# Optimization experiments

Measured on AMD Instinct MI355X. Metric: run time of the kernel, lower is better.

Reference implementation:

```python
import jax, jax.numpy as jnp
import numpy as np

B, S, D, H = 4, 2048, 1024, 16
HD = D // H


def setup_inputs() -> dict:
    key = jax.random.key(0)
    ks = jax.random.split(key, 12)
    sc = 1.0 / np.sqrt(D)
    return {
        "x": jax.random.normal(ks[0], (B, S, D), dtype=jnp.float32),
        "key_padding_mask": jax.random.randint(ks[1], (B, S), 0, 2).astype(bool),
        "attn_mask_modifier": jax.random.uniform(ks[2], (B, S, S), dtype=jnp.float32),
        "Wq": jax.random.normal(ks[3], (D, D), dtype=jnp.float32) * sc,
        "bq": jax.random.normal(ks[4], (D,), dtype=jnp.float32) * sc,
        "Wk": jax.random.normal(ks[5], (D, D), dtype=jnp.float32) * sc,
        "bk": jax.random.normal(ks[6], (D,), dtype=jnp.float32) * sc,
        "Wv": jax.random.normal(ks[7], (D, D), dtype=jnp.float32) * sc,
        "bv": jax.random.normal(ks[8], (D,), dtype=jnp.float32) * sc,
        "Wo": jax.random.normal(ks[9], (D, D), dtype=jnp.float32) * sc,
        "bo": jax.random.normal(ks[10], (D,), dtype=jnp.float32) * sc,
    }


def reference(x, key_padding_mask, attn_mask_modifier, Wq, bq, Wk, bk, Wv, bv, Wo, bo):
    b, s, d = x.shape
    hd = d // H
    # QKV projections -> [b, H, s, hd]
    q = (x @ Wq + bq).reshape(b, s, H, hd).transpose(0, 2, 1, 3)
    k = (x @ Wk + bk).reshape(b, s, H, hd).transpose(0, 2, 1, 3)
    v = (x @ Wv + bv).reshape(b, s, H, hd).transpose(0, 2, 1, 3)
    energy = jnp.einsum("bhqd,bhkd->bhqk", q, k) / jnp.sqrt(jnp.asarray(hd, x.dtype))
    # handle_neg=False path: multiplicative mask modifier, broadcast over heads
    energy = energy * attn_mask_modifier[:, None, :, :]
    # key_padding_mask is applied on the QUERY axis (unsqueeze(1).unsqueeze(-1)) per source
    energy = jnp.where(key_padding_mask[:, None, :, None], jnp.asarray(-1e10, x.dtype), energy)
    attn = jax.nn.softmax(energy, axis=-1)
    out = jnp.einsum("bhqk,bhkd->bhqd", attn, v).transpose(0, 2, 1, 3).reshape(b, s, d)
    return out @ Wo + bo
```

## Files before the change

### kernel.cpp

```cpp
#include <hip/hip_runtime.h>
#include <cstddef>

constexpr int Bn  = 4;
constexpr int Sn  = 2048;
constexpr int Dn  = 1024;
constexpr int Hn  = 16;
constexpr int HDn = 64;

typedef __bf16 bf16;
typedef __attribute__((ext_vector_type(8))) __bf16 bf16x8;
typedef __attribute__((ext_vector_type(4))) __bf16 bf16x4;
typedef __attribute__((ext_vector_type(4))) float  f32x4;

typedef __attribute__((address_space(1))) const void gvoid;
typedef __attribute__((address_space(3))) void lvoid;

__global__ __launch_bounds__(256) void conv_f32_bf16_k(
    const float* __restrict__ in, bf16* __restrict__ out, int n)
{
    int i = (blockIdx.x * 256 + threadIdx.x) * 4;
    if (i + 3 < n) {
        float4 v = *(const float4*)(in + i);
        bf16 o[4] = {(bf16)v.x, (bf16)v.y, (bf16)v.z, (bf16)v.w};
        *(ulong1*)(out + i) = *(ulong1*)o;
    }
}

__global__ __launch_bounds__(256) void bias_cat_k(
    const float* __restrict__ bq, const float* __restrict__ bk,
    const float* __restrict__ bv, float* __restrict__ o)
{
    const int i = blockIdx.x * 256 + threadIdx.x;
    if (i < 1024)      o[i] = bq[i];
    else if (i < 2048) o[i] = bk[i - 1024];
    else if (i < 3072) o[i] = bv[i - 2048];
}

__global__ __launch_bounds__(256) void conv_wt_k(
    const float* __restrict__ w0, const float* __restrict__ w1,
    const float* __restrict__ w2, const float* __restrict__ w3,
    bf16* __restrict__ o0, bf16* __restrict__ o1,
    bf16* __restrict__ o2, bf16* __restrict__ o3)
{
    const float* W = (blockIdx.z == 0) ? w0 : (blockIdx.z == 1) ? w1
                   : (blockIdx.z == 2) ? w2 : w3;
    bf16* O = (blockIdx.z == 0) ? o0 : (blockIdx.z == 1) ? o1
            : (blockIdx.z == 2) ? o2 : o3;
    __shared__ float t[64][65];
    const int tid = threadIdx.x;
    const int k0 = blockIdx.x * 64;
    const int n0 = blockIdx.y * 64;
    #pragma unroll
    for (int p = 0; p < 16; ++p) {
        const int idx = p * 256 + tid;
        const int r = idx >> 6, c = idx & 63;
        t[r][c] = W[(size_t)(k0 + r) * Dn + n0 + c];
    }
    __syncthreads();
    #pragma unroll
    for (int p = 0; p < 16; ++p) {
        const int idx = p * 256 + tid;
        const int r = idx >> 6, c = idx & 63;
        O[(size_t)(n0 + r) * Dn + k0 + c] = (bf16)t[c][r];
    }
}

#define GEMM_STAGE(Ap, Bp, k0, boff)                                          \
    {                                                                         \
        _Pragma("unroll")                                                     \
        for (int j = 0; j < 4; ++j) {                                         \
            const int rbase = (w * 4 + j) * 8;                                \
            const int r = rbase + srow;                                       \
            __builtin_amdgcn_global_load_lds(                                 \
                (gvoid*)(Ap + (size_t)(m0 + r) * Dn + (k0) + scol),           \
                (lvoid*)&smem[(boff) + rbase * 64], 16, 0, 0);                \
            __builtin_amdgcn_global_load_lds(                                 \
                (gvoid*)(Bp + (size_t)(n0 + r) * Dn + (k0) + scol),           \
                (lvoid*)&smem[(boff) + 128 * 64 + rbase * 64], 16, 0, 0);     \
        }                                                                     \
    }

#define GEMM_COMPUTE(boff)                                                    \
    {                                                                         \
        _Pragma("unroll")                                                     \
        for (int ks = 0; ks < 64; ks += 32) {                                 \
            bf16x8 af[4], bfr[4];                                             \
            _Pragma("unroll")                                                 \
            for (int fm = 0; fm < 4; ++fm)                                    \
                af[fm] = *(const bf16x8*)&smem[(boff) +                       \
                    (wm * 64 + fm * 16 + l15) * 64 + ks + quad * 8];          \
            _Pragma("unroll")                                                 \
            for (int fn = 0; fn < 4; ++fn)                                    \
                bfr[fn] = *(const bf16x8*)&smem[(boff) + 128 * 64 +           \
                    (wn * 64 + fn * 16 + l15) * 64 + ks + quad * 8];          \
            _Pragma("unroll")                                                 \
            for (int fm = 0; fm < 4; ++fm)                                    \
                _Pragma("unroll")                                             \
                for (int fn = 0; fn < 4; ++fn)                                \
                    acc[fm][fn] = __builtin_amdgcn_mfma_f32_16x16x32_bf16(    \
                        af[fm], bfr[fn], acc[fm][fn], 0, 0, 0);               \
        }                                                                     \
    }

#define GEMM_KLOOP(Ap, Bp)                                                    \
    GEMM_STAGE(Ap, Bp, 0, 0);                                                 \
    int boff = 0;                                                             \
    for (int kt = 0; kt < Dn / 64; ++kt) {                                    \
        if (kt + 1 < Dn / 64) {                                               \
            GEMM_STAGE(Ap, Bp, (kt + 1) * 64, boff ^ BUF);                    \
            asm volatile("s_waitcnt vmcnt(8)" ::: "memory");                  \
        } else {                                                              \
            asm volatile("s_waitcnt vmcnt(0)" ::: "memory");                  \
        }                                                                     \
        __builtin_amdgcn_s_barrier();                                         \
        __builtin_amdgcn_sched_barrier(0);                                    \
        GEMM_COMPUTE(boff);                                                   \
        __builtin_amdgcn_sched_barrier(0);                                    \
        __builtin_amdgcn_s_barrier();                                         \
        boff ^= BUF;                                                          \
    }

constexpr int BUF = 2 * 128 * 64;

__global__ __launch_bounds__(256) void gemm_out_k(
    const bf16* __restrict__ A, const bf16* __restrict__ Bt,
    const float* __restrict__ bias, float* __restrict__ outv)
{
    __shared__ __align__(16) bf16 smem[2 * BUF];

    const int tid  = threadIdx.x;
    const int w    = tid >> 6;
    const int lane = tid & 63;
    const int quad = lane >> 4;
    const int l15  = lane & 15;
    const int m0   = blockIdx.x * 128;
    const int n0   = blockIdx.y * 128;
    const int wm   = w >> 1;
    const int wn   = w & 1;
    const int srow = lane >> 3;
    const int scol = (lane & 7) * 8;

    f32x4 acc[4][4] = {};

    GEMM_KLOOP(A, Bt);

    #pragma unroll
    for (int fn = 0; fn < 4; ++fn) {
        const int c = n0 + wn * 64 + fn * 16 + l15;
        const float bv = bias[c];
        #pragma unroll
        for (int fm = 0; fm < 4; ++fm)
            #pragma unroll
            for (int i = 0; i < 4; ++i) {
                const int m = m0 + wm * 64 + fm * 16 + quad * 4 + i;
                outv[(size_t)m * Dn + c] = acc[fm][fn][i] + bv;
            }
    }
}

__global__ __launch_bounds__(256) void gemm_qkv_k(
    const bf16* __restrict__ A, const bf16* __restrict__ Wt,
    const float* __restrict__ bias, bf16* __restrict__ qout,
    bf16* __restrict__ kout, bf16* __restrict__ vout, float scq)
{
    __shared__ __align__(16) bf16 smem[2 * BUF];

    const int tid  = threadIdx.x;
    const int w    = tid >> 6;
    const int lane = tid & 63;
    const int quad = lane >> 4;
    const int l15  = lane & 15;
    const int m0   = blockIdx.x * 128;
    const int n0   = blockIdx.y * 128;
    const int wm   = w >> 1;
    const int wn   = w & 1;
    const int srow = lane >> 3;
    const int scol = (lane & 7) * 8;

    f32x4 acc[4][4] = {};

    GEMM_KLOOP(A, Wt);

    const int sec = n0 >> 10;
    const int cb  = n0 & 1023;

    if (sec < 2) {
        bf16* const outp = sec ? kout : qout;
        const float scale = sec ? 1.0f : scq;
        #pragma unroll
        for (int fn = 0; fn < 4; ++fn) {
            const int cc = cb + wn * 64 + fn * 16 + l15;
            const float bv = bias[n0 + wn * 64 + fn * 16 + l15];
            const int h = cc >> 6, hd = cc & 63;
            #pragma unroll
            for (int fm = 0; fm < 4; ++fm)
                #pragma unroll
                for (int i = 0; i < 4; ++i) {
                    const int m = m0 + wm * 64 + fm * 16 + quad * 4 + i;
                    const int b = m >> 11, s = m & (Sn - 1);
                    outp[(((size_t)(b * Hn + h) * Sn) + s) * HDn + hd] =
                        (bf16)((acc[fm][fn][i] + bv) * scale);
                }
        }
    } else {
        bf16* const T = smem;
        #pragma unroll
        for (int fn = 0; fn < 4; ++fn) {
            const int n = wn * 64 + fn * 16 + l15;
            const float bv = bias[n0 + n];
            #pragma unroll
            for (int fm = 0; fm < 4; ++fm) {
                const int m = wm * 64 + fm * 16 + quad * 4;
                bf16x4 pk;
                #pragma unroll
                for (int i = 0; i < 4; ++i)
                    pk[i] = (bf16)(acc[fm][fn][i] + bv);
                *(bf16x4*)&T[n * 136 + m] = pk;
            }
        }
        __syncthreads();
        const int b  = m0 >> 11;
        const int s0 = m0 & (Sn - 1);
        #pragma unroll
        for (int it = 0; it < 8; ++it) {
            const int n    = it * 16 + (tid >> 4);
            const int mcol = (tid & 15) * 8;
            const int gh = (cb + n) >> 6, ghd = (cb + n) & 63;
            bf16x8 v = *(const bf16x8*)&T[n * 136 + mcol];
            *(bf16x8*)(vout +
                (((size_t)(b * Hn + gh) * HDn) + ghd) * Sn + s0 + mcol) = v;
        }
    }
}

__device__ __forceinline__ int sidx(int r, int c) {
    return r * 64 + (c ^ ((r & 7) << 3));
}

__global__ __launch_bounds__(512, 6) void attn_mfma_k(
    const bf16* __restrict__ Qb, const bf16* __restrict__ Kb,
    const bf16* __restrict__ Vtb, const int* __restrict__ kpm,
    const float* __restrict__ mod, bf16* __restrict__ att)
{
    __shared__ __align__(16) bf16 Ks[2][64 * 64];
    __shared__ __align__(16) bf16 Vts[2][64 * 64];
    __shared__ __align__(16) bf16 Ps[128 * 64];

    const int tid  = threadIdx.x;
    const int w    = tid >> 6;
    const int lane = tid & 63;
    const int quad = lane >> 4;
    const int l15  = lane & 15;
    const int blk  = blockIdx.x;
    const int bh   = blk >> 4;
    const int q0   = (blk & 15) * 128;
    const int b    = bh >> 4;
    const int h    = bh & 15;
    const size_t base = (size_t)bh * Sn * HDn;

    const int qrow = q0 + w * 16 + l15;
    const bf16x8 qf0 = *(const bf16x8*)(Qb + base + (size_t)qrow * HDn + 0  + quad * 8);
    const bf16x8 qf1 = *(const bf16x8*)(Qb + base + (size_t)qrow * HDn + 32 + quad * 8);

    const float qbias = (kpm[(size_t)b * Sn + qrow] != 0) ? -1e30f : 0.0f;
    const float* modrow = mod + ((size_t)b * Sn + qrow) * Sn;

    float m_r = -1e30f;
    float l_r = 0.0f;
    f32x4 O[4] = {};

    const int rl = lane >> 3;
    const int cg = ((lane & 7) ^ rl) * 8;
    const int gb = w * 8;

    auto stage = [&](int t, int buf) {
        const int k0 = t * 64;
        __builtin_amdgcn_global_load_lds(
            (gvoid*)(Kb + base + (size_t)(k0 + gb + rl) * HDn + cg),
            (lvoid*)&Ks[buf][gb * 64], 16, 0, 0);
        __builtin_amdgcn_global_load_lds(
            (gvoid*)(Vtb + base + (size_t)(gb + rl) * Sn + k0 + cg),
            (lvoid*)&Vts[buf][gb * 64], 16, 0, 0);
    };

    stage(0, 0);
    float4 md[4];
    #pragma unroll
    for (int ct = 0; ct < 4; ++ct)
        md[ct] = *(const float4*)(modrow + ct * 16 + quad * 4);
    __syncthreads();

    constexpr int NT = Sn / 64;
    for (int t = 0; t < NT; ++t) {
        const int cur = t & 1;

        float4 mdn[4];
        if (t + 1 < NT) {
            stage(t + 1, cur ^ 1);
            #pragma unroll
            for (int ct = 0; ct < 4; ++ct)
                mdn[ct] = *(const float4*)(modrow + (t + 1) * 64 + ct * 16 + quad * 4);
        }

        float e[4][4];
        #pragma unroll
        for (int ct = 0; ct < 4; ++ct) {
            f32x4 s = {};
            #pragma unroll
            for (int ks = 0; ks < 64; ks += 32) {
                bf16x8 kf = *(const bf16x8*)&Ks[cur][sidx(ct * 16 + l15, ks + quad * 8)];
                s = __builtin_amdgcn_mfma_f32_16x16x32_bf16(kf, ks ? qf1 : qf0, s, 0, 0, 0);
            }
            #pragma unroll
            for (int i = 0; i < 4; ++i)
                e[ct][i] = fmaf(s[i], (&md[ct].x)[i], qbias);
        }

        float pm[4];
        #pragma unroll
        for (int ct = 0; ct < 4; ++ct)
            pm[ct] = fmaxf(fmaxf(e[ct][0], e[ct][1]), fmaxf(e[ct][2], e[ct][3]));
        float pmax = fmaxf(fmaxf(pm[0], pm[1]), fmaxf(pm[2], pm[3]));
        pmax = fmaxf(pmax, __shfl_xor(pmax, 16));
        pmax = fmaxf(pmax, __shfl_xor(pmax, 32));

        if (__any(pmax > m_r + 8.0f)) {
            const float mnew  = fmaxf(m_r, pmax);
            const float alpha = __builtin_amdgcn_exp2f(m_r - mnew);
            m_r = mnew;
            l_r *= alpha;
            float aO[4];
            #pragma unroll
            for (int i = 0; i < 4; ++i)
                aO[i] = __shfl(alpha, quad * 4 + i, 16);
            #pragma unroll
            for (int ct = 0; ct < 4; ++ct)
                #pragma unroll
                for (int i = 0; i < 4; ++i)
                    O[ct][i] *= aO[i];
        }

        float rsc[4];
        #pragma unroll
        for (int ct = 0; ct < 4; ++ct) {
            bf16x4 pb;
            float pf[4];
            #pragma unroll
            for (int i = 0; i < 4; ++i) {
                const bf16 p = (bf16)__builtin_amdgcn_exp2f(e[ct][i] - m_r);
                pb[i] = p;
                pf[i] = (float)p;
            }
            rsc[ct] = (pf[0] + pf[1]) + (pf[2] + pf[3]);
            *(bf16x4*)&Ps[sidx(w * 16 + l15, ct * 16 + quad * 4)] = pb;
        }
        float rs = (rsc[0] + rsc[1]) + (rsc[2] + rsc[3]);
        rs += __shfl_xor(rs, 16);
        rs += __shfl_xor(rs, 32);
        l_r += rs;

        #pragma unroll
        for (int ks = 0; ks < 64; ks += 32) {
            bf16x8 paf = *(const bf16x8*)&Ps[sidx(w * 16 + l15, ks + quad * 8)];
            #pragma unroll
            for (int ct = 0; ct < 4; ++ct) {
                bf16x8 vf = *(const bf16x8*)&Vts[cur][sidx(ct * 16 + l15, ks + quad * 8)];
                O[ct] = __builtin_amdgcn_mfma_f32_16x16x32_bf16(paf, vf, O[ct], 0, 0, 0);
            }
        }

        if (t + 1 < NT) {
            #pragma unroll
            for (int ct = 0; ct < 4; ++ct)
                md[ct] = mdn[ct];
        }
        __syncthreads();
    }

    float lO[4];
    #pragma unroll
    for (int i = 0; i < 4; ++i)
        lO[i] = 1.0f / __shfl(l_r, quad * 4 + i, 16);
    #pragma unroll
    for (int ct = 0; ct < 4; ++ct)
        #pragma unroll
        for (int i = 0; i < 4; ++i) {
            const int row = q0 + w * 16 + quad * 4 + i;
            const int col = h * HDn + ct * 16 + l15;
            att[((size_t)b * Sn + row) * Dn + col] = (bf16)(O[ct][i] * lO[i]);
        }
}

extern "C" void kernel_launch(void* const* d_in, const int* in_sizes, int n_in,
                              void* d_out, int out_size, void* d_ws, size_t ws_size,
                              hipStream_t stream) {
    const float* x   = (const float*)d_in[0];
    const int*   kpm = (const int*)d_in[1];
    const float* mod = (const float*)d_in[2];
    const float* Wq  = (const float*)d_in[3];
    const float* bq  = (const float*)d_in[4];
    const float* Wk  = (const float*)d_in[5];
    const float* bk  = (const float*)d_in[6];
    const float* Wv  = (const float*)d_in[7];
    const float* bv  = (const float*)d_in[8];
    const float* Wo  = (const float*)d_in[9];
    const float* bo  = (const float*)d_in[10];
    float* out = (float*)d_out;

    bf16* ws = (bf16*)d_ws;
    const size_t sz = (size_t)Bn * Sn * Dn;
    const size_t wz = (size_t)Dn * Dn;
    bf16* xb   = ws;
    bf16* qb   = ws + sz;
    bf16* kb   = ws + 2 * sz;
    bf16* vtb  = ws + 3 * sz;
    bf16* attb = ws + 4 * sz;
    bf16* wqt  = ws + 5 * sz;
    bf16* wkt  = wqt + wz;
    bf16* wvt  = wkt + wz;
    bf16* wot  = wvt + wz;
    float* bqkv = (float*)(wot + wz);

    conv_f32_bf16_k<<<(int)(sz / 1024), 256, 0, stream>>>(x, xb, (int)sz);
    conv_wt_k<<<dim3(16, 16, 4), 256, 0, stream>>>(Wq, Wk, Wv, Wo, wqt, wkt, wvt, wot);
    bias_cat_k<<<12, 256, 0, stream>>>(bq, bk, bv, bqkv);

    const float SC = 0.125f * 1.44269504088896340736f;

    gemm_qkv_k<<<dim3(64, 24), 256, 0, stream>>>(xb, wqt, bqkv, qb, kb, vtb, SC);

    attn_mfma_k<<<Bn * Hn * (Sn / 128), 512, 0, stream>>>(qb, kb, vtb, kpm, mod, attb);

    gemm_out_k<<<dim3(64, 8), 256, 0, stream>>>(attb, wot, bo, out);
}
```

Baseline: 416.2 us.

## Enlarge projection GEMM tiles to 256x256 with XCD-aware block remapping

```diff
diff --git a/kernel.cpp b/kernel.cpp
--- a/kernel.cpp
+++ b/kernel.cpp
@@ -65,7 +65,7 @@
     }
 }
 
-#define GEMM_STAGE(Ap, Bp, k0, boff)                                          \
+#define GEMM_STAGE256(Ap, Bp, k0)                                             \
     {                                                                         \
         _Pragma("unroll")                                                     \
         for (int j = 0; j < 4; ++j) {                                         \
@@ -73,28 +73,28 @@
             const int r = rbase + srow;                                       \
             __builtin_amdgcn_global_load_lds(                                 \
                 (gvoid*)(Ap + (size_t)(m0 + r) * Dn + (k0) + scol),           \
-                (lvoid*)&smem[(boff) + rbase * 64], 16, 0, 0);                \
+                (lvoid*)&smem[rbase * 64], 16, 0, 0);                         \
             __builtin_amdgcn_global_load_lds(                                 \
                 (gvoid*)(Bp + (size_t)(n0 + r) * Dn + (k0) + scol),           \
-                (lvoid*)&smem[(boff) + 128 * 64 + rbase * 64], 16, 0, 0);     \
+                (lvoid*)&smem[16384 + rbase * 64], 16, 0, 0);                 \
         }                                                                     \
     }
 
-#define GEMM_COMPUTE(boff)                                                    \
+#define GEMM_COMPUTE256                                                       \
     {                                                                         \
         _Pragma("unroll")                                                     \
         for (int ks = 0; ks < 64; ks += 32) {                                 \
-            bf16x8 af[4], bfr[4];                                             \
+            bf16x8 af[8], bfr[4];                                             \
             _Pragma("unroll")                                                 \
-            for (int fm = 0; fm < 4; ++fm)                                    \
-                af[fm] = *(const bf16x8*)&smem[(boff) +                       \
-                    (wm * 64 + fm * 16 + l15) * 64 + ks + quad * 8];          \
+            for (int fm = 0; fm < 8; ++fm)                                    \
+                af[fm] = *(const bf16x8*)&smem[                               \
+                    (wm * 128 + fm * 16 + l15) * 64 + ks + quad * 8];         \
             _Pragma("unroll")                                                 \
             for (int fn = 0; fn < 4; ++fn)                                    \
-                bfr[fn] = *(const bf16x8*)&smem[(boff) + 128 * 64 +           \
+                bfr[fn] = *(const bf16x8*)&smem[16384 +                       \
                     (wn * 64 + fn * 16 + l15) * 64 + ks + quad * 8];          \
             _Pragma("unroll")                                                 \
-            for (int fm = 0; fm < 4; ++fm)                                    \
+            for (int fm = 0; fm < 8; ++fm)                                    \
                 _Pragma("unroll")                                             \
                 for (int fn = 0; fn < 4; ++fn)                                \
                     acc[fm][fn] = __builtin_amdgcn_mfma_f32_16x16x32_bf16(    \
@@ -102,84 +102,74 @@
         }                                                                     \
     }
 
-#define GEMM_KLOOP(Ap, Bp)                                                    \
-    GEMM_STAGE(Ap, Bp, 0, 0);                                                 \
-    int boff = 0;                                                             \
+#define GEMM_KLOOP256(Ap, Bp)                                                 \
     for (int kt = 0; kt < Dn / 64; ++kt) {                                    \
-        if (kt + 1 < Dn / 64) {                                               \
-            GEMM_STAGE(Ap, Bp, (kt + 1) * 64, boff ^ BUF);                    \
-            asm volatile("s_waitcnt vmcnt(8)" ::: "memory");                  \
-        } else {                                                              \
-            asm volatile("s_waitcnt vmcnt(0)" ::: "memory");                  \
-        }                                                                     \
-        __builtin_amdgcn_s_barrier();                                         \
-        __builtin_amdgcn_sched_barrier(0);                                    \
-        GEMM_COMPUTE(boff);                                                   \
-        __builtin_amdgcn_sched_barrier(0);                                    \
-        __builtin_amdgcn_s_barrier();                                         \
-        boff ^= BUF;                                                          \
-    }
-
-constexpr int BUF = 2 * 128 * 64;
-
-__global__ __launch_bounds__(256) void gemm_out_k(
+        GEMM_STAGE256(Ap, Bp, kt * 64);                                       \
+        __syncthreads();                                                      \
+        GEMM_COMPUTE256;                                                      \
+        __syncthreads();                                                      \
+    }
+
+__global__ __launch_bounds__(512) void gemm_out_k(
     const bf16* __restrict__ A, const bf16* __restrict__ Bt,
     const float* __restrict__ bias, float* __restrict__ outv)
 {
-    __shared__ __align__(16) bf16 smem[2 * BUF];
+    __shared__ __align__(16) bf16 smem[2 * 256 * 64];
 
     const int tid  = threadIdx.x;
     const int w    = tid >> 6;
     const int lane = tid & 63;
     const int quad = lane >> 4;
     const int l15  = lane & 15;
-    const int m0   = blockIdx.x * 128;
-    const int n0   = blockIdx.y * 128;
-    const int wm   = w >> 1;
-    const int wn   = w & 1;
+    const int wgid = (blockIdx.x & 7) * 16 + (blockIdx.x >> 3);
+    const int m0   = (wgid >> 2) * 256;
+    const int n0   = (wgid & 3) * 256;
+    const int wm   = w >> 2;
+    const int wn   = w & 3;
     const int srow = lane >> 3;
     const int scol = (lane & 7) * 8;
 
-    f32x4 acc[4][4] = {};
-
-    GEMM_KLOOP(A, Bt);
+    f32x4 acc[8][4] = {};
+
+    GEMM_KLOOP256(A, Bt);
 
     #pragma unroll
     for (int fn = 0; fn < 4; ++fn) {
         const int c = n0 + wn * 64 + fn * 16 + l15;
         const float bv = bias[c];
         #pragma unroll
-        for (int fm = 0; fm < 4; ++fm)
+        for (int fm = 0; fm < 8; ++fm)
             #pragma unroll
             for (int i = 0; i < 4; ++i) {
-                const int m = m0 + wm * 64 + fm * 16 + quad * 4 + i;
+                const int m = m0 + wm * 128 + fm * 16 + quad * 4 + i;
                 outv[(size_t)m * Dn + c] = acc[fm][fn][i] + bv;
             }
     }
 }
 
-__global__ __launch_bounds__(256) void gemm_qkv_k(
+__global__ __launch_bounds__(512) void gemm_qkv_k(
     const bf16* __restrict__ A, const bf16* __restrict__ Wt,
     const float* __restrict__ bias, bf16* __restrict__ qout,
     bf16* __restrict__ kout, bf16* __restrict__ vout, float scq)
 {
-    __shared__ __align__(16) bf16 smem[2 * BUF];
+    __shared__ __align__(16) bf16 smem[2 * 256 * 64];
 
     const int tid  = threadIdx.x;
     const int w    = tid >> 6;
     const int lane = tid & 63;
     const int quad = lane >> 4;
     const int l15  = lane & 15;
-    const int m0   = blockIdx.x * 128;
-    const int n0   = blockIdx.y * 128;
-    const int wm   = w >> 1;
-    const int wn   = w & 1;
+    const int wgid = (blockIdx.x & 7) * 48 + (blockIdx.x >> 3);
+    const int m0   = (wgid / 12) * 256;
+    const int n0   = (wgid % 12) * 256;
+    const int wm   = w >> 2;
+    const int wn   = w & 3;
     const int srow = lane >> 3;
     const int scol = (lane & 7) * 8;
 
-    f32x4 acc[4][4] = {};
-
-    GEMM_KLOOP(A, Wt);
+    f32x4 acc[8][4] = {};
+
+    GEMM_KLOOP256(A, Wt);
 
     const int sec = n0 >> 10;
     const int cb  = n0 & 1023;
@@ -193,10 +183,10 @@
             const float bv = bias[n0 + wn * 64 + fn * 16 + l15];
             const int h = cc >> 6, hd = cc & 63;
             #pragma unroll
-            for (int fm = 0; fm < 4; ++fm)
+            for (int fm = 0; fm < 8; ++fm)
                 #pragma unroll
                 for (int i = 0; i < 4; ++i) {
-                    const int m = m0 + wm * 64 + fm * 16 + quad * 4 + i;
+                    const int m = m0 + wm * 128 + fm * 16 + quad * 4 + i;
                     const int b = m >> 11, s = m & (Sn - 1);
                     outp[(((size_t)(b * Hn + h) * Sn) + s) * HDn + hd] =
                         (bf16)((acc[fm][fn][i] + bv) * scale);
@@ -204,31 +194,38 @@
         }
     } else {
         bf16* const T = smem;
-        #pragma unroll
-        for (int fn = 0; fn < 4; ++fn) {
-            const int n = wn * 64 + fn * 16 + l15;
-            const float bv = bias[n0 + n];
-            #pragma unroll
-            for (int fm = 0; fm < 4; ++fm) {
-                const int m = wm * 64 + fm * 16 + quad * 4;
-                bf16x4 pk;
+        const int b   = m0 >> 11;
+        const int s0  = m0 & (Sn - 1);
+        #pragma unroll
+        for (int r = 0; r < 4; ++r) {
+            if (wn == r) {
                 #pragma unroll
-                for (int i = 0; i < 4; ++i)
-                    pk[i] = (bf16)(acc[fm][fn][i] + bv);
-                *(bf16x4*)&T[n * 136 + m] = pk;
-            }
-        }
-        __syncthreads();
-        const int b  = m0 >> 11;
-        const int s0 = m0 & (Sn - 1);
-        #pragma unroll
-        for (int it = 0; it < 8; ++it) {
-            const int n    = it * 16 + (tid >> 4);
-            const int mcol = (tid & 15) * 8;
-            const int gh = (cb + n) >> 6, ghd = (cb + n) & 63;
-            bf16x8 v = *(const bf16x8*)&T[n * 136 + mcol];
-            *(bf16x8*)(vout +
-                (((size_t)(b * Hn + gh) * HDn) + ghd) * Sn + s0 + mcol) = v;
+                for (int fn = 0; fn < 4; ++fn) {
+                    const int row = fn * 16 + l15;
+                    const float bv = bias[n0 + r * 64 + row];
+                    #pragma unroll
+                    for (int fm = 0; fm < 8; ++fm) {
+                        const int col = wm * 128 + fm * 16 + quad * 4;
+                        bf16x4 pk;
+                        #pragma unroll
+                        for (int i = 0; i < 4; ++i)
+                            pk[i] = (bf16)(acc[fm][fn][i] + bv);
+                        *(bf16x4*)&T[row * 264 + col] = pk;
+                    }
+                }
+            }
+            __syncthreads();
+            #pragma unroll
+            for (int p = 0; p < 4; ++p) {
+                const int row = p * 16 + (tid >> 5);
+                const int col = (tid & 31) * 8;
+                const int rn  = cb + r * 64 + row;
+                const int gh = rn >> 6, ghd = rn & 63;
+                bf16x8 v = *(const bf16x8*)&T[row * 264 + col];
+                *(bf16x8*)(vout +
+                    (((size_t)(b * Hn + gh) * HDn) + ghd) * Sn + s0 + col) = v;
+            }
+            __syncthreads();
         }
     }
 }
@@ -427,9 +424,9 @@
 
     const float SC = 0.125f * 1.44269504088896340736f;
 
-    gemm_qkv_k<<<dim3(64, 24), 256, 0, stream>>>(xb, wqt, bqkv, qb, kb, vtb, SC);
+    gemm_qkv_k<<<384, 512, 0, stream>>>(xb, wqt, bqkv, qb, kb, vtb, SC);
 
     attn_mfma_k<<<Bn * Hn * (Sn / 128), 512, 0, stream>>>(qb, kb, vtb, kpm, mod, attb);
 
-    gemm_out_k<<<dim3(64, 8), 256, 0, stream>>>(attb, wot, bo, out);
-}
+    gemm_out_k<<<128, 512, 0, stream>>>(attb, wot, bo, out);
+}
```

Result: slower. 469.4 us (+12.8%).
